# Kernel optimization log

Measured on AMD Instinct MI355X. Metric: run time of the kernel, lower is better.

Reference implementation:

```python
import jax, jax.numpy as jnp
import numpy as np

VOCAB, P, K, B, L, R = 50257, 512, 64, 32, 2048, 5


def setup_inputs() -> dict:
    key = jax.random.key(0)
    k1, k2, k3, k4, k5, k6, k7 = jax.random.split(key, 7)
    return {
        "x": jax.random.randint(k1, (B, L), 0, VOCAB, dtype=jnp.int32),
        "V": jax.random.normal(k2, (VOCAB, P), dtype=jnp.float32),
        "C": jax.random.normal(k3, (K, P), dtype=jnp.float32),
        "f1_w": jax.random.normal(k4, (2 * R + 1,), dtype=jnp.float32),
        "f1_b": jax.random.normal(k5, (K,), dtype=jnp.float32),
        "f2_w": jax.random.normal(k6, (K, P), dtype=jnp.float32),
        "f2_b": jax.random.normal(k7, (K,), dtype=jnp.float32),
    }


def reference(x, V, C, f1_w, f1_b, f2_w, f2_b):
    b, l = x.shape
    k, p = C.shape
    w = f1_w.shape[0]
    r = (w - 1) // 2
    emb = V[x]                                              # [B,L,P] embedding lookup
    x_hat = emb / jnp.linalg.norm(emb, axis=2, keepdims=True)
    l_hat = C / jnp.linalg.norm(C, axis=1, keepdims=True)
    G = jnp.einsum('kp,blp->bkl', l_hat, x_hat)             # cosine sim [B,K,L]
    # sliding-window dot product == depthwise 1D cross-correlation, 'same' padding
    u = jax.lax.conv_general_dilated(
        G.reshape(b * k, 1, l), f1_w.reshape(1, 1, w),
        window_strides=(1,), padding=[(r, r)],
        dimension_numbers=('NCH', 'OIH', 'NCH'),
    ).reshape(b, k, l)
    m = jax.nn.relu(u + f1_b[None, :, None])                # [B,K,L]
    beta = jax.nn.softmax(m.max(axis=1), axis=1)            # max over labels, softmax over seq -> [B,L]
    pooled = jnp.mean(beta[:, :, None] * emb, axis=1)       # [B,P]
    return pooled @ f2_w.T + f2_b                           # [B,K]
```

## Files before the change

### kernel.cpp

```cpp
#include <hip/hip_runtime.h>
#include <hip/hip_bf16.h>

#define PP     512
#define KK     64
#define BB     32
#define LLEN   2048
#define NPOS   (BB * LLEN)

typedef __attribute__((ext_vector_type(8)))  short short8;
typedef __attribute__((ext_vector_type(16))) float float16;

__device__ inline unsigned int pack_bf2(float lo, float hi) {
    __hip_bfloat162 h = __float22bfloat162_rn(make_float2(lo, hi));
    unsigned int u;
    __builtin_memcpy(&u, &h, 4);
    return u;
}
__device__ inline float bf_lo(unsigned int v) { return __uint_as_float(v << 16); }
__device__ inline float bf_hi(unsigned int v) { return __uint_as_float(v & 0xffff0000u); }

__global__ void k1_prep(const float* __restrict__ C, const float* __restrict__ f2w,
                        ushort* __restrict__ Bu) {
    const int n = blockIdx.x;
    const float* src = (n < 64) ? (C + n * PP) : (f2w + (n - 64) * PP);
    const int t = threadIdx.x;
    float v0 = src[t];
    float v1 = src[t + 256];
    __shared__ float red[256];
    red[t] = v0 * v0 + v1 * v1;
    __syncthreads();
    for (int s = 128; s > 0; s >>= 1) {
        if (t < s) red[t] += red[t + s];
        __syncthreads();
    }
    const float inv = (n < 64) ? rsqrtf(red[0]) : 1.f;
    Bu[(((t >> 3)       * 128 + n) << 3) + (t & 7)] = (ushort)(pack_bf2(v0 * inv, 0.f) & 0xffffu);
    Bu[((((t + 256) >> 3)) * 128 + n) * 8 + (t & 7)] = (ushort)(pack_bf2(v1 * inv, 0.f) & 0xffffu);
}

__launch_bounds__(256)
__global__ void k2_gemm(const int* __restrict__ x, const float* __restrict__ V,
                        const uint4* __restrict__ Bu4,
                        unsigned int* __restrict__ Gt2, unsigned int* __restrict__ E2p) {
    __shared__ uint4 sA[64 * 64];
    __shared__ int   stok[64];
    __shared__ float rnorm[64];

    const int tid  = threadIdx.x;
    const int lane = tid & 63;
    const int wv   = tid >> 6;
    const int r    = tid >> 2;
    const int q    = tid & 3;

    if (tid < 64) stok[tid] = x[blockIdx.x * 64 + tid];
    __syncthreads();

    const float* src = V + (size_t)stok[r] * PP + q * 4;
    const int swzr = r & 7;
    float nrm = 0.f;

    float4 pa[16];
#pragma unroll
    for (int g = 0; g < 16; ++g) pa[g] = ((const float4*)src)[g * 4];
    float4 pb[16];
#pragma unroll
    for (int g = 0; g < 16; ++g) pb[g] = ((const float4*)src)[(g + 16) * 4];

#pragma unroll
    for (int g = 0; g < 16; ++g) {
        const float4 a = pa[g];
        nrm = fmaf(a.x, a.x, fmaf(a.y, a.y, fmaf(a.z, a.z, fmaf(a.w, a.w, nrm))));
        uint2 w2; w2.x = pack_bf2(a.x, a.y); w2.y = pack_bf2(a.z, a.w);
        const int f = g * 2 + (q >> 1);
        ((uint2*)&sA[r * 64 + (f ^ swzr)])[q & 1] = w2;
    }
#pragma unroll
    for (int g = 0; g < 16; ++g) {
        const float4 a = pb[g];
        nrm = fmaf(a.x, a.x, fmaf(a.y, a.y, fmaf(a.z, a.z, fmaf(a.w, a.w, nrm))));
        uint2 w2; w2.x = pack_bf2(a.x, a.y); w2.y = pack_bf2(a.z, a.w);
        const int f = (g + 16) * 2 + (q >> 1);
        ((uint2*)&sA[r * 64 + (f ^ swzr)])[q & 1] = w2;
    }

    nrm += __shfl_xor(nrm, 1, 64);
    nrm += __shfl_xor(nrm, 2, 64);
    if (q == 0) rnorm[r] = rsqrtf(nrm);
    __syncthreads();

    float16 acc0, acc1;
#pragma unroll
    for (int i = 0; i < 16; ++i) { acc0[i] = 0.f; acc1[i] = 0.f; }

    const int mt  = (wv & 1) * 32;
    const int nh  = (wv >> 1) * 64;
    const int l31 = lane & 31;
    const int cc  = lane >> 5;
    const int mq  = mt + l31;
    const int abase = mq * 64;
    const int aswz  = mq & 7;

#pragma unroll 8
    for (int ks = 0; ks < 32; ++ks) {
        const int ff = ks * 2 + cc;
        const uint4 av = sA[abase + (ff ^ aswz)];
        const uint4 b0 = Bu4[ff * 128 + nh + l31];
        const uint4 b1 = Bu4[ff * 128 + nh + 32 + l31];
        short8 a8, t0, t1;
        __builtin_memcpy(&a8, &av, 16);
        __builtin_memcpy(&t0, &b0, 16);
        __builtin_memcpy(&t1, &b1, 16);
        acc0 = __builtin_amdgcn_mfma_f32_32x32x16_bf16(a8, t0, acc0, 0, 0, 0);
        acc1 = __builtin_amdgcn_mfma_f32_32x32x16_bf16(a8, t1, acc1, 0, 0, 0);
    }

    const size_t posBase = (size_t)blockIdx.x * 64;
#pragma unroll
    for (int reg = 0; reg < 16; ++reg) {
        const int rr = (reg & 3) + 8 * (reg >> 2) + 4 * (lane >> 5);
        const int m  = mt + rr;
        const size_t p = posBase + m;
        if (wv < 2) {
            const float rn = rnorm[m];
            Gt2[p * 32 + l31] = pack_bf2(acc0[reg] * rn, acc1[reg] * rn);
        } else {
            E2p[p * 32 + l31] = pack_bf2(acc0[reg], acc1[reg]);
        }
    }
}

__global__ void k3_convpool(const unsigned int* __restrict__ Gt2,
                            const unsigned int* __restrict__ E2p,
                            const float* __restrict__ f1w, const float* __restrict__ f1b,
                            float* __restrict__ pool) {
    __shared__ unsigned int sT[74 * 33];
    __shared__ float smv[64];
    __shared__ float sp[64];
    __shared__ float sscal[2];
    __shared__ float sred[8][64];

    const int b  = blockIdx.x >> 5;
    const int l0 = (blockIdx.x & 31) * 64;
    const int t  = threadIdx.x;

    for (int idx = t; idx < 74 * 32; idx += 256) {
        const int row = idx >> 5, col = idx & 31;
        const int gl = l0 - 5 + row;
        sT[row * 33 + col] = (gl >= 0 && gl < LLEN)
            ? Gt2[((size_t)b * LLEN + gl) * 32 + col] : 0u;
    }
    __syncthreads();

    float w[11];
#pragma unroll
    for (int j = 0; j < 11; ++j) w[j] = f1w[j];
    const int j = t & 31;
    const int h = t >> 5;
    const float bias0 = f1b[j], bias1 = f1b[j + 32];
#pragma unroll
    for (int i = 0; i < 8; ++i) {
        const int lr = i * 8 + h;
        float u0 = 0.f, u1 = 0.f;
#pragma unroll
        for (int tap = 0; tap < 11; ++tap) {
            const unsigned int v = sT[(lr + tap) * 33 + j];
            u0 = fmaf(bf_lo(v), w[tap], u0);
            u1 = fmaf(bf_hi(v), w[tap], u1);
        }
        float m = fmaxf(fmaxf(u0 + bias0, 0.f), fmaxf(u1 + bias1, 0.f));
#pragma unroll
        for (int off = 16; off > 0; off >>= 1)
            m = fmaxf(m, __shfl_xor(m, off, 64));
        if (j == 0) smv[lr] = m;
    }
    __syncthreads();

    if (t < 64) {
        float v = smv[t];
#pragma unroll
        for (int off = 32; off > 0; off >>= 1)
            v = fmaxf(v, __shfl_xor(v, off, 64));
        if (t == 0) sscal[0] = v;
    }
    __syncthreads();
    const float mx = sscal[0];
    if (t < 64) sp[t] = __expf(smv[t] - mx);
    __syncthreads();
    if (t < 64) {
        float s = sp[t];
#pragma unroll
        for (int off = 32; off > 0; off >>= 1)
            s += __shfl_xor(s, off, 64);
        if (t == 0) sscal[1] = s;
    }

    float a0 = 0.f, a1 = 0.f;
#pragma unroll
    for (int i = 0; i < 8; ++i) {
        const int l = i * 8 + h;
        const float wgt = sp[l];
        const unsigned int e = E2p[((size_t)b * LLEN + l0 + l) * 32 + j];
        a0 = fmaf(wgt, bf_lo(e), a0);
        a1 = fmaf(wgt, bf_hi(e), a1);
    }
    sred[h][j]      = a0;
    sred[h][j + 32] = a1;
    __syncthreads();
    if (t < 64) {
        float r = 0.f;
#pragma unroll
        for (int hh = 0; hh < 8; ++hh) r += sred[hh][t];
        float* dst = pool + (size_t)blockIdx.x * 68;
        dst[t] = r;
        if (t == 0) { dst[64] = sscal[0]; dst[65] = sscal[1]; }
    }
}

__global__ void k6_final(const float* __restrict__ pool, const float* __restrict__ f2b,
                         float* __restrict__ out) {
    const int b = blockIdx.x;
    const int k = threadIdx.x;
    float M = -1e30f;
#pragma unroll
    for (int c = 0; c < 32; ++c)
        M = fmaxf(M, pool[(size_t)(b * 32 + c) * 68 + 64]);
    float tot = 0.f, num = 0.f;
#pragma unroll
    for (int c = 0; c < 32; ++c) {
        const float* pc = pool + (size_t)(b * 32 + c) * 68;
        const float sc = __expf(pc[64] - M);
        tot = fmaf(sc, pc[65], tot);
        num = fmaf(sc, pc[k], num);
    }
    out[b * KK + k] = (num / tot) * (1.f / 2048.f) + f2b[k];
}

extern "C" void kernel_launch(void* const* d_in, const int* in_sizes, int n_in,
                              void* d_out, int out_size, void* d_ws, size_t ws_size,
                              hipStream_t stream) {
    const int*   x   = (const int*)d_in[0];
    const float* V   = (const float*)d_in[1];
    const float* C   = (const float*)d_in[2];
    const float* f1w = (const float*)d_in[3];
    const float* f1b = (const float*)d_in[4];
    const float* f2w = (const float*)d_in[5];
    const float* f2b = (const float*)d_in[6];
    float* out = (float*)d_out;

    float* ws = (float*)d_ws;
    ushort* Bu = (ushort*)ws;
    unsigned int* Gt2 = (unsigned int*)(ws + 32768);
    unsigned int* E2p = Gt2 + (size_t)NPOS * 32;
    float* pool = (float*)(E2p + (size_t)NPOS * 32);

    k1_prep    <<<128, 256, 0, stream>>>(C, f2w, Bu);
    k2_gemm    <<<NPOS / 64, 256, 0, stream>>>(x, V, (const uint4*)Bu, Gt2, E2p);
    k3_convpool<<<BB * 32, 256, 0, stream>>>(Gt2, E2p, f1w, f1b, pool);
    k6_final   <<<BB, 64, 0, stream>>>(pool, f2b, out);
}
```

Baseline: 191.1 us.

## Fuse embedding GEMM with conv and softmax pooling, recomputing halo rows in-block

Merges the gather+MFMA GEMM kernel with the conv/softmax/pool kernel so each block gathers 74 embedding rows (64 positions plus a 5-row halo on each side), computes cosine sims and f2 projections in registers, and stages them in shared memory instead of global Gt2/E2p buffers. This removes the global round trip of the intermediate tensors and one kernel launch. The cost is recomputing the halo rows per block (about 16% extra gather and GEMM work) and an uneven wave workload, since one wave runs two tiles.

```diff
diff --git a/kernel.cpp b/kernel.cpp
--- a/kernel.cpp
+++ b/kernel.cpp
@@ -5,7 +5,7 @@
 #define KK     64
 #define BB     32
 #define LLEN   2048
-#define NPOS   (BB * LLEN)
+#define SROWS  74
 
 typedef __attribute__((ext_vector_type(8)))  short short8;
 typedef __attribute__((ext_vector_type(16))) float float16;
@@ -38,132 +38,171 @@
     Bu[((((t + 256) >> 3)) * 128 + n) * 8 + (t & 7)] = (ushort)(pack_bf2(v1 * inv, 0.f) & 0xffffu);
 }
 
-__launch_bounds__(256)
-__global__ void k2_gemm(const int* __restrict__ x, const float* __restrict__ V,
-                        const uint4* __restrict__ Bu4,
-                        unsigned int* __restrict__ Gt2, unsigned int* __restrict__ E2p) {
-    __shared__ uint4 sA[64 * 64];
-    __shared__ int   stok[64];
-    __shared__ float rnorm[64];
-
-    const int tid  = threadIdx.x;
-    const int lane = tid & 63;
-    const int wv   = tid >> 6;
-    const int r    = tid >> 2;
-    const int q    = tid & 3;
-
-    if (tid < 64) stok[tid] = x[blockIdx.x * 64 + tid];
-    __syncthreads();
-
-    const float* src = V + (size_t)stok[r] * PP + q * 4;
-    const int swzr = r & 7;
-    float nrm = 0.f;
-
-    float4 pa[16];
-#pragma unroll
-    for (int g = 0; g < 16; ++g) pa[g] = ((const float4*)src)[g * 4];
-    float4 pb[16];
-#pragma unroll
-    for (int g = 0; g < 16; ++g) pb[g] = ((const float4*)src)[(g + 16) * 4];
-
-#pragma unroll
-    for (int g = 0; g < 16; ++g) {
-        const float4 a = pa[g];
-        nrm = fmaf(a.x, a.x, fmaf(a.y, a.y, fmaf(a.z, a.z, fmaf(a.w, a.w, nrm))));
-        uint2 w2; w2.x = pack_bf2(a.x, a.y); w2.y = pack_bf2(a.z, a.w);
-        const int f = g * 2 + (q >> 1);
-        ((uint2*)&sA[r * 64 + (f ^ swzr)])[q & 1] = w2;
-    }
-#pragma unroll
-    for (int g = 0; g < 16; ++g) {
-        const float4 a = pb[g];
-        nrm = fmaf(a.x, a.x, fmaf(a.y, a.y, fmaf(a.z, a.z, fmaf(a.w, a.w, nrm))));
-        uint2 w2; w2.x = pack_bf2(a.x, a.y); w2.y = pack_bf2(a.z, a.w);
-        const int f = (g + 16) * 2 + (q >> 1);
-        ((uint2*)&sA[r * 64 + (f ^ swzr)])[q & 1] = w2;
-    }
-
-    nrm += __shfl_xor(nrm, 1, 64);
-    nrm += __shfl_xor(nrm, 2, 64);
-    if (q == 0) rnorm[r] = rsqrtf(nrm);
-    __syncthreads();
-
-    float16 acc0, acc1;
-#pragma unroll
-    for (int i = 0; i < 16; ++i) { acc0[i] = 0.f; acc1[i] = 0.f; }
-
-    const int mt  = (wv & 1) * 32;
-    const int nh  = (wv >> 1) * 64;
-    const int l31 = lane & 31;
-    const int cc  = lane >> 5;
-    const int mq  = mt + l31;
-    const int abase = mq * 64;
-    const int aswz  = mq & 7;
-
-#pragma unroll 8
-    for (int ks = 0; ks < 32; ++ks) {
-        const int ff = ks * 2 + cc;
-        const uint4 av = sA[abase + (ff ^ aswz)];
-        const uint4 b0 = Bu4[ff * 128 + nh + l31];
-        const uint4 b1 = Bu4[ff * 128 + nh + 32 + l31];
-        short8 a8, t0, t1;
-        __builtin_memcpy(&a8, &av, 16);
-        __builtin_memcpy(&t0, &b0, 16);
-        __builtin_memcpy(&t1, &b1, 16);
-        acc0 = __builtin_amdgcn_mfma_f32_32x32x16_bf16(a8, t0, acc0, 0, 0, 0);
-        acc1 = __builtin_amdgcn_mfma_f32_32x32x16_bf16(a8, t1, acc1, 0, 0, 0);
-    }
-
-    const size_t posBase = (size_t)blockIdx.x * 64;
-#pragma unroll
-    for (int reg = 0; reg < 16; ++reg) {
-        const int rr = (reg & 3) + 8 * (reg >> 2) + 4 * (lane >> 5);
-        const int m  = mt + rr;
-        const size_t p = posBase + m;
-        if (wv < 2) {
-            const float rn = rnorm[m];
-            Gt2[p * 32 + l31] = pack_bf2(acc0[reg] * rn, acc1[reg] * rn);
-        } else {
-            E2p[p * 32 + l31] = pack_bf2(acc0[reg], acc1[reg]);
-        }
-    }
-}
-
-__global__ void k3_convpool(const unsigned int* __restrict__ Gt2,
-                            const unsigned int* __restrict__ E2p,
-                            const float* __restrict__ f1w, const float* __restrict__ f1b,
-                            float* __restrict__ pool) {
-    __shared__ unsigned int sT[74 * 33];
+__launch_bounds__(256, 2)
+__global__ void k2_fused(const int* __restrict__ x, const float* __restrict__ V,
+                         const uint4* __restrict__ Bu4,
+                         const float* __restrict__ f1w, const float* __restrict__ f1b,
+                         float* __restrict__ pool) {
+    __shared__ uint4 sA[SROWS * 64];
+    __shared__ int   stok[SROWS];
+    __shared__ float rnorm[SROWS];
     __shared__ float smv[64];
     __shared__ float sp[64];
     __shared__ float sscal[2];
     __shared__ float sred[8][64];
 
-    const int b  = blockIdx.x >> 5;
-    const int l0 = (blockIdx.x & 31) * 64;
-    const int t  = threadIdx.x;
-
-    for (int idx = t; idx < 74 * 32; idx += 256) {
-        const int row = idx >> 5, col = idx & 31;
-        const int gl = l0 - 5 + row;
-        sT[row * 33 + col] = (gl >= 0 && gl < LLEN)
-            ? Gt2[((size_t)b * LLEN + gl) * 32 + col] : 0u;
+    const int tid  = threadIdx.x;
+    const int lane = tid & 63;
+    const int wv   = tid >> 6;
+    const int l31  = lane & 31;
+    const int b    = blockIdx.x >> 5;
+    const int l0   = (blockIdx.x & 31) * 64;
+
+    if (tid < SROWS) {
+        int gl = l0 - 5 + tid;
+        gl = min(max(gl, 0), LLEN - 1);
+        stok[tid] = x[b * LLEN + gl];
+    }
+    __syncthreads();
+
+    const int q = tid & 3;
+    {
+        const int r    = tid >> 2;
+        const float* src = V + (size_t)stok[r] * PP + q * 4;
+        const int swzr = r & 7;
+        float nrm = 0.f;
+        float4 pa[16];
+#pragma unroll
+        for (int g = 0; g < 16; ++g) pa[g] = ((const float4*)src)[g * 4];
+        float4 pb[16];
+#pragma unroll
+        for (int g = 0; g < 16; ++g) pb[g] = ((const float4*)src)[(g + 16) * 4];
+#pragma unroll
+        for (int g = 0; g < 16; ++g) {
+            const float4 a = pa[g];
+            nrm = fmaf(a.x, a.x, fmaf(a.y, a.y, fmaf(a.z, a.z, fmaf(a.w, a.w, nrm))));
+            uint2 w2; w2.x = pack_bf2(a.x, a.y); w2.y = pack_bf2(a.z, a.w);
+            const int f = g * 2 + (q >> 1);
+            ((uint2*)&sA[r * 64 + (f ^ swzr)])[q & 1] = w2;
+        }
+#pragma unroll
+        for (int g = 0; g < 16; ++g) {
+            const float4 a = pb[g];
+            nrm = fmaf(a.x, a.x, fmaf(a.y, a.y, fmaf(a.z, a.z, fmaf(a.w, a.w, nrm))));
+            uint2 w2; w2.x = pack_bf2(a.x, a.y); w2.y = pack_bf2(a.z, a.w);
+            const int f = (g + 16) * 2 + (q >> 1);
+            ((uint2*)&sA[r * 64 + (f ^ swzr)])[q & 1] = w2;
+        }
+        nrm += __shfl_xor(nrm, 1, 64);
+        nrm += __shfl_xor(nrm, 2, 64);
+        if (q == 0) rnorm[r] = rsqrtf(nrm);
+    }
+    if (tid < 40) {
+        const int r    = 64 + (tid >> 2);
+        const float* src = V + (size_t)stok[r] * PP + q * 4;
+        const int swzr = r & 7;
+        float nrm = 0.f;
+        float4 pa[16];
+#pragma unroll
+        for (int g = 0; g < 16; ++g) pa[g] = ((const float4*)src)[g * 4];
+        float4 pb[16];
+#pragma unroll
+        for (int g = 0; g < 16; ++g) pb[g] = ((const float4*)src)[(g + 16) * 4];
+#pragma unroll
+        for (int g = 0; g < 16; ++g) {
+            const float4 a = pa[g];
+            nrm = fmaf(a.x, a.x, fmaf(a.y, a.y, fmaf(a.z, a.z, fmaf(a.w, a.w, nrm))));
+            uint2 w2; w2.x = pack_bf2(a.x, a.y); w2.y = pack_bf2(a.z, a.w);
+            const int f = g * 2 + (q >> 1);
+            ((uint2*)&sA[r * 64 + (f ^ swzr)])[q & 1] = w2;
+        }
+#pragma unroll
+        for (int g = 0; g < 16; ++g) {
+            const float4 a = pb[g];
+            nrm = fmaf(a.x, a.x, fmaf(a.y, a.y, fmaf(a.z, a.z, fmaf(a.w, a.w, nrm))));
+            uint2 w2; w2.x = pack_bf2(a.x, a.y); w2.y = pack_bf2(a.z, a.w);
+            const int f = (g + 16) * 2 + (q >> 1);
+            ((uint2*)&sA[r * 64 + (f ^ swzr)])[q & 1] = w2;
+        }
+        nrm += __shfl_xor(nrm, 1, 64);
+        nrm += __shfl_xor(nrm, 2, 64);
+        if (q == 0) rnorm[r] = rsqrtf(nrm);
+    }
+    __syncthreads();
+
+    float16 c0, c1, d0, d1;
+#pragma unroll
+    for (int i = 0; i < 16; ++i) { c0[i] = 0.f; c1[i] = 0.f; d0[i] = 0.f; d1[i] = 0.f; }
+
+    auto tile = [&](int rowBase, int nh, float16& A0, float16& A1) {
+        const int cc    = lane >> 5;
+        const int row   = rowBase + l31;
+        const int abase = row * 64;
+        const int aswz  = row & 7;
+#pragma unroll 8
+        for (int ks = 0; ks < 32; ++ks) {
+            const int ff = ks * 2 + cc;
+            const uint4 av = sA[abase + (ff ^ aswz)];
+            const uint4 b0 = Bu4[ff * 128 + nh + l31];
+            const uint4 b1 = Bu4[ff * 128 + nh + 32 + l31];
+            short8 a8, t0, t1;
+            __builtin_memcpy(&a8, &av, 16);
+            __builtin_memcpy(&t0, &b0, 16);
+            __builtin_memcpy(&t1, &b1, 16);
+            A0 = __builtin_amdgcn_mfma_f32_32x32x16_bf16(a8, t0, A0, 0, 0, 0);
+            A1 = __builtin_amdgcn_mfma_f32_32x32x16_bf16(a8, t1, A1, 0, 0, 0);
+        }
+    };
+    if      (wv == 0) { tile(0, 0, c0, c1); }
+    else if (wv == 1) { tile(32, 0, c0, c1); }
+    else if (wv == 2) { tile(42, 0, c0, c1); tile(37, 64, d0, d1); }
+    else              { tile(5, 64, d0, d1); }
+    __syncthreads();
+
+    unsigned int* G32 = (unsigned int*)sA;
+    float*        E2s = (float*)((char*)sA + 10240);
+    const int cc = lane >> 5;
+    if (wv < 3) {
+        const int rowBase = (wv == 0) ? 0 : (wv == 1) ? 32 : 42;
+#pragma unroll
+        for (int reg = 0; reg < 16; ++reg) {
+            const int rr  = (reg & 3) + 8 * (reg >> 2) + 4 * cc;
+            const int row = rowBase + rr;
+            if (wv == 2 && row < 64) continue;
+            const int gl = l0 - 5 + row;
+            unsigned int vpk = 0u;
+            if (gl >= 0 && gl < LLEN) {
+                const float rn = rnorm[row];
+                vpk = pack_bf2(c0[reg] * rn, c1[reg] * rn);
+            }
+            G32[row * 32 + l31] = vpk;
+        }
+    }
+    if (wv >= 2) {
+        const int rowBase = (wv == 2) ? 37 : 5;
+#pragma unroll
+        for (int reg = 0; reg < 16; ++reg) {
+            const int rr = (reg & 3) + 8 * (reg >> 2) + 4 * cc;
+            const int o  = rowBase - 5 + rr;
+            E2s[o * 64 + l31]      = d0[reg];
+            E2s[o * 64 + 32 + l31] = d1[reg];
+        }
     }
     __syncthreads();
 
     float w[11];
 #pragma unroll
-    for (int j = 0; j < 11; ++j) w[j] = f1w[j];
-    const int j = t & 31;
-    const int h = t >> 5;
+    for (int t = 0; t < 11; ++t) w[t] = f1w[t];
+    const int j = l31;
+    const int h = tid >> 5;
     const float bias0 = f1b[j], bias1 = f1b[j + 32];
 #pragma unroll
     for (int i = 0; i < 8; ++i) {
-        const int lr = i * 8 + h;
+        const int o = i * 8 + h;
         float u0 = 0.f, u1 = 0.f;
 #pragma unroll
         for (int tap = 0; tap < 11; ++tap) {
-            const unsigned int v = sT[(lr + tap) * 33 + j];
+            const unsigned int v = G32[(o + tap) * 32 + j];
             u0 = fmaf(bf_lo(v), w[tap], u0);
             u1 = fmaf(bf_hi(v), w[tap], u1);
         }
@@ -171,48 +210,47 @@
 #pragma unroll
         for (int off = 16; off > 0; off >>= 1)
             m = fmaxf(m, __shfl_xor(m, off, 64));
-        if (j == 0) smv[lr] = m;
-    }
-    __syncthreads();
-
-    if (t < 64) {
-        float v = smv[t];
+        if (j == 0) smv[o] = m;
+    }
+    __syncthreads();
+
+    if (tid < 64) {
+        float v = smv[tid];
 #pragma unroll
         for (int off = 32; off > 0; off >>= 1)
             v = fmaxf(v, __shfl_xor(v, off, 64));
-        if (t == 0) sscal[0] = v;
+        if (tid == 0) sscal[0] = v;
     }
     __syncthreads();
     const float mx = sscal[0];
-    if (t < 64) sp[t] = __expf(smv[t] - mx);
-    __syncthreads();
-    if (t < 64) {
-        float s = sp[t];
+    if (tid < 64) sp[tid] = __expf(smv[tid] - mx);
+    __syncthreads();
+    if (tid < 64) {
+        float s = sp[tid];
 #pragma unroll
         for (int off = 32; off > 0; off >>= 1)
             s += __shfl_xor(s, off, 64);
-        if (t == 0) sscal[1] = s;
+        if (tid == 0) sscal[1] = s;
     }
 
     float a0 = 0.f, a1 = 0.f;
 #pragma unroll
     for (int i = 0; i < 8; ++i) {
-        const int l = i * 8 + h;
-        const float wgt = sp[l];
-        const unsigned int e = E2p[((size_t)b * LLEN + l0 + l) * 32 + j];
-        a0 = fmaf(wgt, bf_lo(e), a0);
-        a1 = fmaf(wgt, bf_hi(e), a1);
+        const int o = i * 8 + h;
+        const float wgt = sp[o];
+        a0 = fmaf(wgt, E2s[o * 64 + j], a0);
+        a1 = fmaf(wgt, E2s[o * 64 + 32 + j], a1);
     }
     sred[h][j]      = a0;
     sred[h][j + 32] = a1;
     __syncthreads();
-    if (t < 64) {
+    if (tid < 64) {
         float r = 0.f;
 #pragma unroll
-        for (int hh = 0; hh < 8; ++hh) r += sred[hh][t];
+        for (int hh = 0; hh < 8; ++hh) r += sred[hh][tid];
         float* dst = pool + (size_t)blockIdx.x * 68;
-        dst[t] = r;
-        if (t == 0) { dst[64] = sscal[0]; dst[65] = sscal[1]; }
+        dst[tid] = r;
+        if (tid == 0) { dst[64] = sscal[0]; dst[65] = sscal[1]; }
     }
 }
 
@@ -249,12 +287,9 @@
 
     float* ws = (float*)d_ws;
     ushort* Bu = (ushort*)ws;
-    unsigned int* Gt2 = (unsigned int*)(ws + 32768);
-    unsigned int* E2p = Gt2 + (size_t)NPOS * 32;
-    float* pool = (float*)(E2p + (size_t)NPOS * 32);
-
-    k1_prep    <<<128, 256, 0, stream>>>(C, f2w, Bu);
-    k2_gemm    <<<NPOS / 64, 256, 0, stream>>>(x, V, (const uint4*)Bu, Gt2, E2p);
-    k3_convpool<<<BB * 32, 256, 0, stream>>>(Gt2, E2p, f1w, f1b, pool);
-    k6_final   <<<BB, 64, 0, stream>>>(pool, f2b, out);
-}
+    float* pool = ws + 32768;
+
+    k1_prep <<<128, 256, 0, stream>>>(C, f2w, Bu);
+    k2_fused<<<BB * 32, 256, 0, stream>>>(x, V, (const uint4*)Bu, f1w, f1b, pool);
+    k6_final<<<BB, 64, 0, stream>>>(pool, f2b, out);
+}
```

Result: no change. 192.9 us (+0.9%).
